# Optimization experiments

Hardware: AMD Instinct MI355X
Metric: run time of the kernel (lower is better)

Reference implementation:

```python
import jax, jax.numpy as jnp
import numpy as np

B, T, I, H, A = 128, 1024, 128, 256, 40


def setup_inputs() -> dict:
    key = jax.random.key(0)
    ks = jax.random.split(key, 10)
    s_ih = 1.0 / np.sqrt(H)
    return {
        "x": jax.random.normal(ks[0], (B, T, I), dtype=jnp.float32),
        "W_ih": jax.random.uniform(ks[1], (3 * H, I), minval=-s_ih, maxval=s_ih, dtype=jnp.float32),
        "W_hh": jax.random.uniform(ks[2], (3 * H, H), minval=-s_ih, maxval=s_ih, dtype=jnp.float32),
        "b_ih": jax.random.uniform(ks[3], (3 * H,), minval=-s_ih, maxval=s_ih, dtype=jnp.float32),
        "b_hh": jax.random.uniform(ks[4], (3 * H,), minval=-s_ih, maxval=s_ih, dtype=jnp.float32),
        "wv_W": jax.random.normal(ks[5], (A, H), dtype=jnp.float32) * 0.05,
        "wv_b": jnp.zeros((A,), dtype=jnp.float32),
        "wu": jax.random.uniform(ks[6], (A,), dtype=jnp.float32),
        "h2o_W": jax.random.normal(ks[7], (1, H), dtype=jnp.float32) * 0.05,
        "h2o_b": jnp.zeros((1,), dtype=jnp.float32),
    }


def _gru_outputs(x, W_ih, W_hh, b_ih, b_hh):
    # Precompute input-side gate projections for all timesteps: [B,T,3H]
    gx = jnp.einsum("bti,gi->btg", x, W_ih) + b_ih
    h0 = jnp.zeros((x.shape[0], H), dtype=x.dtype)

    def step(h, gx_t):
        gh = h @ W_hh.T + b_hh                      # [B,3H]
        xr, xz, xn = jnp.split(gx_t, 3, axis=-1)    # torch gate order r,z,n
        hr, hz, hn = jnp.split(gh, 3, axis=-1)
        r = jax.nn.sigmoid(xr + hr)
        z = jax.nn.sigmoid(xz + hz)
        n = jnp.tanh(xn + r * hn)
        h_new = (1.0 - z) * n + z * h
        return h_new, h_new

    _, hs = jax.lax.scan(step, h0, jnp.swapaxes(gx, 0, 1))  # hs: [T,B,H]
    return jnp.swapaxes(hs, 0, 1)  # [B,T,H]


def reference(x, W_ih, W_hh, b_ih, b_hh, wv_W, wv_b, wu, h2o_W, h2o_b):
    outputs = _gru_outputs(x, W_ih, W_hh, b_ih, b_hh)          # [B,T,H]
    um = jnp.tanh(jnp.einsum("bth,ah->bta", outputs, wv_W) + wv_b)  # [B,T,A]
    alpha = jax.nn.softmax(um @ wu, axis=1)                    # [B,T]
    context = jnp.einsum("bt,bth->bh", alpha, outputs)         # [B,H]
    # dropout_layer is identity in eval mode
    out = context @ h2o_W.T + h2o_b                            # [B,1]
    return out
```

## Files before the change

### kernel.cpp

```cpp
#include <hip/hip_runtime.h>


#define B_ 128
#define T_ 1024
#define I_ 128
#define H_ 256
#define G_ 768
#define A_ 40

typedef _Float16 f16;
typedef _Float16 f16x2 __attribute__((ext_vector_type(2)));

__device__ __forceinline__ float fdot2(unsigned a, unsigned b, float c){
#if __has_builtin(__builtin_amdgcn_fdot2)
  return __builtin_amdgcn_fdot2(__builtin_bit_cast(f16x2, a),
                                __builtin_bit_cast(f16x2, b), c, false);
#else
  f16x2 av = __builtin_bit_cast(f16x2, a), bv = __builtin_bit_cast(f16x2, b);
  return c + (float)av.x * (float)bv.x + (float)av.y * (float)bv.y;
#endif
}

__device__ __forceinline__ float2 h2f(unsigned u){
  f16x2 h = __builtin_bit_cast(f16x2, u);
  return make_float2((float)h.x, (float)h.y);
}
__device__ __forceinline__ unsigned f2h2(float a, float b){
  f16x2 h; h.x = (f16)a; h.y = (f16)b;
  return __builtin_bit_cast(unsigned, h);
}
__device__ __forceinline__ float sigm_(float x){ return 1.f / (1.f + __expf(-x)); }
__device__ __forceinline__ float tanh_(float x){ return 1.f - 2.f / (__expf(2.f * x) + 1.f); }

__global__ __launch_bounds__(256) void k_prep_w(const float* __restrict__ W,
                                                unsigned* __restrict__ Wp){
  int idx = blockIdx.x * 256 + threadIdx.x;
  int d   = idx >> 9;
  int col = idx & 511;
  int g = col >> 1, sub = col & 1;
  int c = d >> 6, p = d & 63;
  int r = g + 256 * c;
  int k = sub * 128 + 2 * p;
  Wp[(size_t)d * 512 + col] = f2h2(W[r * 256 + k], W[r * 256 + k + 1]);
}

__global__ __launch_bounds__(256) void k_gx(const float* __restrict__ x,
                                            const float* __restrict__ wih,
                                            const float* __restrict__ bih,
                                            unsigned* __restrict__ gx){
  __shared__ float Al[64 * 68];
  __shared__ float Bl[64 * 68];
  const int tid = threadIdx.x;
  const int m0 = blockIdx.x * 64, n0 = blockIdx.y * 64;
  const int ar = tid >> 4, bc = tid & 15;
  float acc[4][4] = {{0.f}};

  for (int kh = 0; kh < 2; ++kh){
    __syncthreads();
    #pragma unroll
    for (int u = 0; u < 4; ++u){
      int idx = tid + 256 * u;
      int row = idx >> 4;
      int kq  = idx & 15;
      float4 va = *(const float4*)(x   + (size_t)(m0 + row) * I_ + kh * 64 + kq * 4);
      float4 vb = *(const float4*)(wih + (size_t)(n0 + row) * I_ + kh * 64 + kq * 4);
      Al[(kq*4+0)*68 + row] = va.x; Al[(kq*4+1)*68 + row] = va.y;
      Al[(kq*4+2)*68 + row] = va.z; Al[(kq*4+3)*68 + row] = va.w;
      Bl[(kq*4+0)*68 + row] = vb.x; Bl[(kq*4+1)*68 + row] = vb.y;
      Bl[(kq*4+2)*68 + row] = vb.z; Bl[(kq*4+3)*68 + row] = vb.w;
    }
    __syncthreads();
    for (int k = 0; k < 64; ++k){
      float4 a4 = *(const float4*)(Al + k * 68 + ar * 4);
      float4 b4 = *(const float4*)(Bl + k * 68 + bc * 4);
      acc[0][0] += a4.x*b4.x; acc[0][1] += a4.x*b4.y; acc[0][2] += a4.x*b4.z; acc[0][3] += a4.x*b4.w;
      acc[1][0] += a4.y*b4.x; acc[1][1] += a4.y*b4.y; acc[1][2] += a4.y*b4.z; acc[1][3] += a4.y*b4.w;
      acc[2][0] += a4.z*b4.x; acc[2][1] += a4.z*b4.y; acc[2][2] += a4.z*b4.z; acc[2][3] += a4.z*b4.w;
      acc[3][0] += a4.w*b4.x; acc[3][1] += a4.w*b4.y; acc[3][2] += a4.w*b4.z; acc[3][3] += a4.w*b4.w;
    }
  }

  float bn[4];
  #pragma unroll
  for (int j = 0; j < 4; ++j) bn[j] = bih[n0 + bc * 4 + j];
  #pragma unroll
  for (int i = 0; i < 4; ++i){
    int m = m0 + ar * 4 + i;
    uint2 st;
    st.x = f2h2(acc[i][0] + bn[0], acc[i][1] + bn[1]);
    st.y = f2h2(acc[i][2] + bn[2], acc[i][3] + bn[3]);
    *(uint2*)(gx + (size_t)m * (G_ / 2) + n0 / 2 + bc * 2) = st;
  }
}

__global__ __launch_bounds__(512, 2) void k_gru(const unsigned* __restrict__ Wp,
                                                unsigned* __restrict__ gx,
                                                const float* __restrict__ bhh,
                                                int unused){
  __shared__ uint4 HB4[2][32];
  const int tid = threadIdx.x;
  const int b = blockIdx.x;
  const int g = tid >> 1, sub = tid & 1;

  unsigned w[192];
  #pragma unroll
  for (int d = 0; d < 192; ++d) w[d] = Wp[d * 512 + tid];

  float br = 0.f, bz = 0.f, bn_ = 0.f, hprev = 0.f;
  if (sub == 0){ br = bhh[g]; bz = bhh[H_ + g]; bn_ = bhh[2 * H_ + g]; }
  if (tid < 32) HB4[0][tid] = make_uint4(0, 0, 0, 0);
  __syncthreads();

  f16* gxp = (f16*)gx + (size_t)b * T_ * G_;

  float xr = 0.f, xz = 0.f, xn = 0.f;
  if (sub == 0){ xr = (float)gxp[g]; xz = (float)gxp[H_ + g]; xn = (float)gxp[2 * H_ + g]; }

  int buf = 0;
  for (int t = 0; t < T_; ++t){
    float nr = 0.f, nz = 0.f, nn = 0.f;
    if (sub == 0 && t < T_ - 1){
      const f16* nx = gxp + (size_t)(t + 1) * G_;
      nr = (float)nx[g]; nz = (float)nx[H_ + g]; nn = (float)nx[2 * H_ + g];
    }

    float a0 = 0.f, a1 = 0.f, a2 = 0.f;
    #pragma unroll
    for (int i = 0; i < 16; ++i){
      uint4 hc = HB4[buf][sub * 16 + i];
      a0 = fdot2(w[      i*4+0], hc.x, a0); a0 = fdot2(w[      i*4+1], hc.y, a0);
      a0 = fdot2(w[      i*4+2], hc.z, a0); a0 = fdot2(w[      i*4+3], hc.w, a0);
      a1 = fdot2(w[ 64 + i*4+0], hc.x, a1); a1 = fdot2(w[ 64 + i*4+1], hc.y, a1);
      a1 = fdot2(w[ 64 + i*4+2], hc.z, a1); a1 = fdot2(w[ 64 + i*4+3], hc.w, a1);
      a2 = fdot2(w[128 + i*4+0], hc.x, a2); a2 = fdot2(w[128 + i*4+1], hc.y, a2);
      a2 = fdot2(w[128 + i*4+2], hc.z, a2); a2 = fdot2(w[128 + i*4+3], hc.w, a2);
    }
    a0 += __shfl_xor(a0, 1);
    a1 += __shfl_xor(a1, 1);
    a2 += __shfl_xor(a2, 1);

    if (sub == 0){
      float rg = sigm_(xr + a0 + br);
      float zg = sigm_(xz + a1 + bz);
      float ng = tanh_(xn + rg * (a2 + bn_));
      float hn = (1.f - zg) * ng + zg * hprev;
      hprev = hn;
      f16 hh = (f16)hn;
      ((f16*)HB4[buf ^ 1])[g] = hh;
      gxp[(size_t)t * G_ + g] = hh;
      xr = nr; xz = nz; xn = nn;
    }
    __syncthreads();
    buf ^= 1;
  }
}

__global__ __launch_bounds__(256) void k_score(const f16* __restrict__ outs,
                                               const float* __restrict__ wvW,
                                               const float* __restrict__ wvb,
                                               const float* __restrict__ wu,
                                               float* __restrict__ s){
  __shared__ uint4 OT[32 * 33];
  __shared__ float WV[A_ * 260];
  const int tid = threadIdx.x;
  const int m0 = blockIdx.x * 32;

  #pragma unroll
  for (int u = 0; u < 4; ++u){
    int idx = tid + 256 * u;
    int row = idx >> 5, col = idx & 31;
    OT[row * 33 + col] = *(const uint4*)(outs + (size_t)(m0 + row) * G_ + col * 8);
  }
  #pragma unroll
  for (int u = 0; u < 10; ++u){
    int f = tid + 256 * u;
    int a = f >> 6, k4 = f & 63;
    float4 v = *(const float4*)(wvW + a * 256 + k4 * 4);
    *(float4*)(WV + a * 260 + k4 * 4) = v;
  }
  __syncthreads();

  const int m = tid >> 3, aq = tid & 7;
  float acc[5] = {0.f, 0.f, 0.f, 0.f, 0.f};
  for (int i = 0; i < 32; ++i){
    uint4 oc = OT[m * 33 + i];
    float2 o01 = h2f(oc.x), o23 = h2f(oc.y), o45 = h2f(oc.z), o67 = h2f(oc.w);
    #pragma unroll
    for (int sa = 0; sa < 5; ++sa){
      int a = aq + sa * 8;
      const float* wr = &WV[a * 260 + i * 8];
      float4 w0 = *(const float4*)wr;
      float4 w1 = *(const float4*)(wr + 4);
      acc[sa] += o01.x*w0.x + o01.y*w0.y + o23.x*w0.z + o23.y*w0.w
               + o45.x*w1.x + o45.y*w1.y + o67.x*w1.z + o67.y*w1.w;
    }
  }
  float sp = 0.f;
  #pragma unroll
  for (int sa = 0; sa < 5; ++sa){
    int a = aq + sa * 8;
    sp += wu[a] * tanh_(acc[sa] + wvb[a]);
  }
  sp += __shfl_xor(sp, 1);
  sp += __shfl_xor(sp, 2);
  sp += __shfl_xor(sp, 4);
  if (aq == 0) s[m0 + m] = sp;
}

__global__ __launch_bounds__(256) void k_ctx(const f16* __restrict__ outs,
                                             const float* __restrict__ s,
                                             const float* __restrict__ h2oW,
                                             const float* __restrict__ h2ob,
                                             float* __restrict__ out){
  __shared__ float AL[T_];
  __shared__ float red[8];
  const int tid = threadIdx.x;
  const int b = blockIdx.x;
  const float* sb = s + (size_t)b * T_;

  float v0 = sb[tid], v1 = sb[tid + 256], v2 = sb[tid + 512], v3 = sb[tid + 768];
  float mx = fmaxf(fmaxf(v0, v1), fmaxf(v2, v3));
  #pragma unroll
  for (int msk = 1; msk < 64; msk <<= 1) mx = fmaxf(mx, __shfl_xor(mx, msk));
  if ((tid & 63) == 0) red[tid >> 6] = mx;
  __syncthreads();
  mx = fmaxf(fmaxf(red[0], red[1]), fmaxf(red[2], red[3]));

  float e0 = __expf(v0 - mx), e1 = __expf(v1 - mx), e2 = __expf(v2 - mx), e3 = __expf(v3 - mx);
  float zs = e0 + e1 + e2 + e3;
  #pragma unroll
  for (int msk = 1; msk < 64; msk <<= 1) zs += __shfl_xor(zs, msk);
  if ((tid & 63) == 0) red[4 + (tid >> 6)] = zs;
  __syncthreads();
  float invZ = 1.f / (red[4] + red[5] + red[6] + red[7]);
  AL[tid] = e0 * invZ; AL[tid + 256] = e1 * invZ;
  AL[tid + 512] = e2 * invZ; AL[tid + 768] = e3 * invZ;
  __syncthreads();

  const f16* ob = outs + (size_t)b * T_ * G_;
  float acc = 0.f;
  for (int t = 0; t < T_; t += 4){
    acc += AL[t + 0] * (float)ob[(size_t)(t + 0) * G_ + tid];
    acc += AL[t + 1] * (float)ob[(size_t)(t + 1) * G_ + tid];
    acc += AL[t + 2] * (float)ob[(size_t)(t + 2) * G_ + tid];
    acc += AL[t + 3] * (float)ob[(size_t)(t + 3) * G_ + tid];
  }
  __syncthreads();
  float val = acc * h2oW[tid];
  #pragma unroll
  for (int msk = 1; msk < 64; msk <<= 1) val += __shfl_xor(val, msk);
  if ((tid & 63) == 0) red[tid >> 6] = val;
  __syncthreads();
  if (tid == 0) out[b] = red[0] + red[1] + red[2] + red[3] + h2ob[0];
}

extern "C" void kernel_launch(void* const* d_in, const int* in_sizes, int n_in,
                              void* d_out, int out_size, void* d_ws, size_t ws_size,
                              hipStream_t stream){
  const float* x    = (const float*)d_in[0];
  const float* wih  = (const float*)d_in[1];
  const float* whh  = (const float*)d_in[2];
  const float* bih  = (const float*)d_in[3];
  const float* bhh  = (const float*)d_in[4];
  const float* wvW  = (const float*)d_in[5];
  const float* wvb  = (const float*)d_in[6];
  const float* wu   = (const float*)d_in[7];
  const float* h2oW = (const float*)d_in[8];
  const float* h2ob = (const float*)d_in[9];
  float* out = (float*)d_out;

  char* ws = (char*)d_ws;
  float*    s  = (float*)ws;
  unsigned* Wp = (unsigned*)(ws + 524288);
  unsigned* gx = (unsigned*)(ws + 917504);

  k_prep_w<<<384, 256, 0, stream>>>(whh, Wp);
  k_gx<<<dim3((B_ * T_) / 64, G_ / 64), 256, 0, stream>>>(x, wih, bih, gx);
  k_gru<<<B_, 512, 0, stream>>>(Wp, gx, bhh, 0);
  k_score<<<(B_ * T_) / 32, 256, 0, stream>>>((const f16*)gx, wvW, wvb, wu, s);
  k_ctx<<<B_, 256, 0, stream>>>((const f16*)gx, s, h2oW, h2ob, out);
}
```

Baseline: 1.999 ms.

## Use MFMA for input projection and tighten GRU recurrent loop

The input-gate projection GEMM moves from scalar FP32 FMAs to fp16 MFMA 16x16x32 instructions. Its LDS tiles are XOR-swizzled, the output is staged through LDS for coalesced stores, and the r/z recurrent biases are folded into the precomputed gates. The recurrent kernel splits each dot product into two accumulator chains for more ILP, swaps the shuffle reduction for a DPP swap, and pads the hidden-state LDS buffer to avoid bank conflicts. Converting x and W_ih to fp16 before the GEMM adds rounding error on the gate inputs.

```diff
diff --git a/kernel.cpp b/kernel.cpp
--- a/kernel.cpp
+++ b/kernel.cpp
@@ -10,6 +10,8 @@
 
 typedef _Float16 f16;
 typedef _Float16 f16x2 __attribute__((ext_vector_type(2)));
+typedef _Float16 f16x8 __attribute__((ext_vector_type(8)));
+typedef float    f32x4 __attribute__((ext_vector_type(4)));
 
 __device__ __forceinline__ float fdot2(unsigned a, unsigned b, float c){
 #if __has_builtin(__builtin_amdgcn_fdot2)
@@ -32,126 +34,169 @@
 __device__ __forceinline__ float sigm_(float x){ return 1.f / (1.f + __expf(-x)); }
 __device__ __forceinline__ float tanh_(float x){ return 1.f - 2.f / (__expf(2.f * x) + 1.f); }
 
+__device__ __forceinline__ float xor1_sum(float x){
+  int xi = __builtin_bit_cast(int, x);
+  int sw = __builtin_amdgcn_update_dpp(0, xi, 0xB1, 0xF, 0xF, true);
+  return x + __builtin_bit_cast(float, sw);
+}
+
 __global__ __launch_bounds__(256) void k_prep_w(const float* __restrict__ W,
                                                 unsigned* __restrict__ Wp){
   int idx = blockIdx.x * 256 + threadIdx.x;
-  int d   = idx >> 9;
+  int dd  = idx >> 9;
   int col = idx & 511;
+  int c = dd >> 6, d = dd & 63;
   int g = col >> 1, sub = col & 1;
-  int c = d >> 6, p = d & 63;
-  int r = g + 256 * c;
-  int k = sub * 128 + 2 * p;
-  Wp[(size_t)d * 512 + col] = f2h2(W[r * 256 + k], W[r * 256 + k + 1]);
+  int r = c * 256 + g;
+  int k = sub * 128 + 2 * d;
+  Wp[(size_t)dd * 512 + col] = f2h2(W[r * 256 + k], W[r * 256 + k + 1]);
 }
 
 __global__ __launch_bounds__(256) void k_gx(const float* __restrict__ x,
                                             const float* __restrict__ wih,
                                             const float* __restrict__ bih,
-                                            unsigned* __restrict__ gx){
-  __shared__ float Al[64 * 68];
-  __shared__ float Bl[64 * 68];
+                                            const float* __restrict__ bhh,
+                                            f16* __restrict__ gx){
+  __shared__ __align__(16) f16 XA[128 * 128];
+  __shared__ __align__(16) f16 XB[64 * 128];
   const int tid = threadIdx.x;
-  const int m0 = blockIdx.x * 64, n0 = blockIdx.y * 64;
-  const int ar = tid >> 4, bc = tid & 15;
-  float acc[4][4] = {{0.f}};
-
-  for (int kh = 0; kh < 2; ++kh){
-    __syncthreads();
-    #pragma unroll
-    for (int u = 0; u < 4; ++u){
-      int idx = tid + 256 * u;
-      int row = idx >> 4;
-      int kq  = idx & 15;
-      float4 va = *(const float4*)(x   + (size_t)(m0 + row) * I_ + kh * 64 + kq * 4);
-      float4 vb = *(const float4*)(wih + (size_t)(n0 + row) * I_ + kh * 64 + kq * 4);
-      Al[(kq*4+0)*68 + row] = va.x; Al[(kq*4+1)*68 + row] = va.y;
-      Al[(kq*4+2)*68 + row] = va.z; Al[(kq*4+3)*68 + row] = va.w;
-      Bl[(kq*4+0)*68 + row] = vb.x; Bl[(kq*4+1)*68 + row] = vb.y;
-      Bl[(kq*4+2)*68 + row] = vb.z; Bl[(kq*4+3)*68 + row] = vb.w;
-    }
-    __syncthreads();
-    for (int k = 0; k < 64; ++k){
-      float4 a4 = *(const float4*)(Al + k * 68 + ar * 4);
-      float4 b4 = *(const float4*)(Bl + k * 68 + bc * 4);
-      acc[0][0] += a4.x*b4.x; acc[0][1] += a4.x*b4.y; acc[0][2] += a4.x*b4.z; acc[0][3] += a4.x*b4.w;
-      acc[1][0] += a4.y*b4.x; acc[1][1] += a4.y*b4.y; acc[1][2] += a4.y*b4.z; acc[1][3] += a4.y*b4.w;
-      acc[2][0] += a4.z*b4.x; acc[2][1] += a4.z*b4.y; acc[2][2] += a4.z*b4.z; acc[2][3] += a4.z*b4.w;
-      acc[3][0] += a4.w*b4.x; acc[3][1] += a4.w*b4.y; acc[3][2] += a4.w*b4.z; acc[3][3] += a4.w*b4.w;
+  const int m0 = blockIdx.x * 128, n0 = blockIdx.y * 64;
+
+  #pragma unroll
+  for (int u = 0; u < 16; ++u){
+    int idx = tid + 256 * u;
+    int row = idx >> 5, k4 = idx & 31;
+    float4 v = *(const float4*)(x + (size_t)(m0 + row) * I_ + k4 * 4);
+    unsigned byte = (unsigned)(row * 256 + k4 * 8) ^ ((row & 7) << 4);
+    *(uint2*)((char*)XA + byte) = make_uint2(f2h2(v.x, v.y), f2h2(v.z, v.w));
+  }
+  #pragma unroll
+  for (int u = 0; u < 8; ++u){
+    int idx = tid + 256 * u;
+    int row = idx >> 5, k4 = idx & 31;
+    float4 v = *(const float4*)(wih + (size_t)(n0 + row) * I_ + k4 * 4);
+    unsigned byte = (unsigned)(row * 256 + k4 * 8) ^ ((row & 7) << 4);
+    *(uint2*)((char*)XB + byte) = make_uint2(f2h2(v.x, v.y), f2h2(v.z, v.w));
+  }
+  __syncthreads();
+
+  const int l = tid & 63, w = tid >> 6;
+  const int q = l >> 4, m16 = l & 15;
+  f32x4 acc[2][4];
+  #pragma unroll
+  for (int i = 0; i < 2; ++i)
+    #pragma unroll
+    for (int nt = 0; nt < 4; ++nt) acc[i][nt] = (f32x4){0.f, 0.f, 0.f, 0.f};
+
+  #pragma unroll
+  for (int kt = 0; kt < 4; ++kt){
+    f16x8 af[2];
+    #pragma unroll
+    for (int i = 0; i < 2; ++i){
+      int row = (2 * w + i) * 16 + m16;
+      unsigned byte = (unsigned)(row * 256 + kt * 64 + q * 16) ^ ((row & 7) << 4);
+      af[i] = *(const f16x8*)((const char*)XA + byte);
+    }
+    #pragma unroll
+    for (int nt = 0; nt < 4; ++nt){
+      int row = nt * 16 + m16;
+      unsigned byte = (unsigned)(row * 256 + kt * 64 + q * 16) ^ ((row & 7) << 4);
+      f16x8 bv = *(const f16x8*)((const char*)XB + byte);
+      acc[0][nt] = __builtin_amdgcn_mfma_f32_16x16x32_f16(af[0], bv, acc[0][nt], 0, 0, 0);
+      acc[1][nt] = __builtin_amdgcn_mfma_f32_16x16x32_f16(af[1], bv, acc[1][nt], 0, 0, 0);
     }
   }
 
   float bn[4];
   #pragma unroll
-  for (int j = 0; j < 4; ++j) bn[j] = bih[n0 + bc * 4 + j];
-  #pragma unroll
-  for (int i = 0; i < 4; ++i){
-    int m = m0 + ar * 4 + i;
-    uint2 st;
-    st.x = f2h2(acc[i][0] + bn[0], acc[i][1] + bn[1]);
-    st.y = f2h2(acc[i][2] + bn[2], acc[i][3] + bn[3]);
-    *(uint2*)(gx + (size_t)m * (G_ / 2) + n0 / 2 + bc * 2) = st;
+  for (int nt = 0; nt < 4; ++nt){
+    int n = n0 + nt * 16 + m16;
+    bn[nt] = bih[n] + (n < 512 ? bhh[n] : 0.f);
+  }
+
+  __syncthreads();
+  f16* ST = XA;
+  #pragma unroll
+  for (int i = 0; i < 2; ++i)
+    #pragma unroll
+    for (int nt = 0; nt < 4; ++nt)
+      #pragma unroll
+      for (int j = 0; j < 4; ++j){
+        int row = (2 * w + i) * 16 + 4 * q + j;
+        ST[row * 72 + nt * 16 + m16] = (f16)(acc[i][nt][j] + bn[nt]);
+      }
+  __syncthreads();
+  #pragma unroll
+  for (int u = 0; u < 4; ++u){
+    int idx = tid + 256 * u;
+    int row = idx >> 3, c = idx & 7;
+    uint4 v = *(const uint4*)(ST + row * 72 + c * 8);
+    *(uint4*)(gx + (size_t)(m0 + row) * G_ + n0 + c * 8) = v;
   }
 }
 
 __global__ __launch_bounds__(512, 2) void k_gru(const unsigned* __restrict__ Wp,
                                                 unsigned* __restrict__ gx,
-                                                const float* __restrict__ bhh,
-                                                int unused){
-  __shared__ uint4 HB4[2][32];
+                                                const float* __restrict__ bhh){
+  __shared__ uint4 hb[2][36];
   const int tid = threadIdx.x;
+  const int g = tid >> 1, sub = tid & 1;
   const int b = blockIdx.x;
-  const int g = tid >> 1, sub = tid & 1;
-
-  unsigned w[192];
-  #pragma unroll
-  for (int d = 0; d < 192; ++d) w[d] = Wp[d * 512 + tid];
-
-  float br = 0.f, bz = 0.f, bn_ = 0.f, hprev = 0.f;
-  if (sub == 0){ br = bhh[g]; bz = bhh[H_ + g]; bn_ = bhh[2 * H_ + g]; }
-  if (tid < 32) HB4[0][tid] = make_uint4(0, 0, 0, 0);
-  __syncthreads();
+
+  unsigned w0[64], w1[64], w2[64];
+  #pragma unroll
+  for (int d = 0; d < 64; ++d) w0[d] = Wp[(size_t)(d      ) * 512 + tid];
+  #pragma unroll
+  for (int d = 0; d < 64; ++d) w1[d] = Wp[(size_t)(64  + d) * 512 + tid];
+  #pragma unroll
+  for (int d = 0; d < 64; ++d) w2[d] = Wp[(size_t)(128 + d) * 512 + tid];
+
+  const float bn_ = bhh[512 + g];
+  float hprev = 0.f;
+  if (tid < 36) hb[0][tid] = make_uint4(0, 0, 0, 0);
 
   f16* gxp = (f16*)gx + (size_t)b * T_ * G_;
-
   float xr = 0.f, xz = 0.f, xn = 0.f;
   if (sub == 0){ xr = (float)gxp[g]; xz = (float)gxp[H_ + g]; xn = (float)gxp[2 * H_ + g]; }
-
-  int buf = 0;
+  __syncthreads();
+
+  const int rb = sub * 18;
+  int cur = 0;
   for (int t = 0; t < T_; ++t){
-    float nr = 0.f, nz = 0.f, nn = 0.f;
-    if (sub == 0 && t < T_ - 1){
+    float pr = 0.f, pz = 0.f, pn = 0.f;
+    if (sub == 0 && t + 1 < T_){
       const f16* nx = gxp + (size_t)(t + 1) * G_;
-      nr = (float)nx[g]; nz = (float)nx[H_ + g]; nn = (float)nx[2 * H_ + g];
-    }
-
-    float a0 = 0.f, a1 = 0.f, a2 = 0.f;
+      pr = (float)nx[g]; pz = (float)nx[H_ + g]; pn = (float)nx[2 * H_ + g];
+    }
+
+    float a00 = 0.f, a01 = 0.f, a10 = 0.f, a11 = 0.f, a20 = 0.f, a21 = 0.f;
     #pragma unroll
     for (int i = 0; i < 16; ++i){
-      uint4 hc = HB4[buf][sub * 16 + i];
-      a0 = fdot2(w[      i*4+0], hc.x, a0); a0 = fdot2(w[      i*4+1], hc.y, a0);
-      a0 = fdot2(w[      i*4+2], hc.z, a0); a0 = fdot2(w[      i*4+3], hc.w, a0);
-      a1 = fdot2(w[ 64 + i*4+0], hc.x, a1); a1 = fdot2(w[ 64 + i*4+1], hc.y, a1);
-      a1 = fdot2(w[ 64 + i*4+2], hc.z, a1); a1 = fdot2(w[ 64 + i*4+3], hc.w, a1);
-      a2 = fdot2(w[128 + i*4+0], hc.x, a2); a2 = fdot2(w[128 + i*4+1], hc.y, a2);
-      a2 = fdot2(w[128 + i*4+2], hc.z, a2); a2 = fdot2(w[128 + i*4+3], hc.w, a2);
-    }
-    a0 += __shfl_xor(a0, 1);
-    a1 += __shfl_xor(a1, 1);
-    a2 += __shfl_xor(a2, 1);
+      uint4 hv = hb[cur][rb + i];
+      a00 = fdot2(w0[4*i+0], hv.x, a00); a01 = fdot2(w0[4*i+1], hv.y, a01);
+      a00 = fdot2(w0[4*i+2], hv.z, a00); a01 = fdot2(w0[4*i+3], hv.w, a01);
+      a10 = fdot2(w1[4*i+0], hv.x, a10); a11 = fdot2(w1[4*i+1], hv.y, a11);
+      a10 = fdot2(w1[4*i+2], hv.z, a10); a11 = fdot2(w1[4*i+3], hv.w, a11);
+      a20 = fdot2(w2[4*i+0], hv.x, a20); a21 = fdot2(w2[4*i+1], hv.y, a21);
+      a20 = fdot2(w2[4*i+2], hv.z, a20); a21 = fdot2(w2[4*i+3], hv.w, a21);
+    }
+    float ar = xor1_sum(a00 + a01);
+    float az = xor1_sum(a10 + a11);
+    float an = xor1_sum(a20 + a21);
 
     if (sub == 0){
-      float rg = sigm_(xr + a0 + br);
-      float zg = sigm_(xz + a1 + bz);
-      float ng = tanh_(xn + rg * (a2 + bn_));
-      float hn = (1.f - zg) * ng + zg * hprev;
-      hprev = hn;
-      f16 hh = (f16)hn;
-      ((f16*)HB4[buf ^ 1])[g] = hh;
+      float rg = sigm_(xr + ar);
+      float zg = sigm_(xz + az);
+      float ng = tanh_(xn + rg * (an + bn_));
+      float h  = (1.f - zg) * ng + zg * hprev;
+      hprev = h;
+      f16 hh = (f16)h;
+      ((f16*)hb[cur ^ 1])[g + (g >> 7) * 16] = hh;
       gxp[(size_t)t * G_ + g] = hh;
-      xr = nr; xz = nz; xn = nn;
+      xr = pr; xz = pz; xn = pn;
     }
     __syncthreads();
-    buf ^= 1;
+    cur ^= 1;
   }
 }
 
@@ -275,8 +320,8 @@
   unsigned* gx = (unsigned*)(ws + 917504);
 
   k_prep_w<<<384, 256, 0, stream>>>(whh, Wp);
-  k_gx<<<dim3((B_ * T_) / 64, G_ / 64), 256, 0, stream>>>(x, wih, bih, gx);
-  k_gru<<<B_, 512, 0, stream>>>(Wp, gx, bhh, 0);
+  k_gx<<<dim3((B_ * T_) / 128, G_ / 64), 256, 0, stream>>>(x, wih, bih, bhh, (f16*)gx);
+  k_gru<<<B_, 512, 0, stream>>>(Wp, gx, bhh);
   k_score<<<(B_ * T_) / 32, 256, 0, stream>>>((const f16*)gx, wvW, wvb, wu, s);
   k_ctx<<<B_, 256, 0, stream>>>((const f16*)gx, s, h2oW, h2ob, out);
 }
```

Result: faster. 1.708 ms (-14.5%).
